# Performance work log

Measured on AMD Instinct MI355X. Metric: run time of the kernel, lower is better.

The kernel has to match this reference:

```python
import jax, jax.numpy as jnp
import numpy as np

B, H, W = 8, 64, 64
C = 256
NUM_HEADS = 8
HEAD_DIM = C // NUM_HEADS  # 32
K0, K1 = 7, 13  # two neighborhood kernel sizes (dilation = 1)


def _starts(L, K):
    """NATTEN (dilation=1) window start and relative-bias start per position."""
    nh = K // 2
    i = jnp.arange(L)
    win = jnp.maximum(i - nh, 0) + jnp.where(i + nh >= L, L - i - nh - 1, 0)
    pb = nh + jnp.where(i < nh, nh - i, 0) + jnp.where(i + nh >= L, L - i - 1 - nh, 0)
    return win, pb


def _na2d(q, k, v, rpb, K):
    """2D neighborhood attention with relative positional bias.
    q,k,v: [B,h,H,W,D] (q pre-scaled); rpb: [h, 2K-1, 2K-1]."""
    Bq, h, Hq, Wq, D = q.shape
    sh, ph = _starts(Hq, K)
    sw, pw = _starts(Wq, K)
    kk = jnp.arange(K)
    idx_h = sh[:, None] + kk            # [H,K] neighbor row indices
    idx_w = sw[:, None] + kk            # [W,K] neighbor col indices
    rows = ph[:, None] + kk             # [H,K] rpb row offsets
    cols = pw[:, None] + kk             # [W,K] rpb col offsets
    # bias[hd,i,ki,j,kj] = rpb[hd, rows[i,ki], cols[j,kj]] -> [h,H,K,W,K]
    bias = rpb[:, rows[:, :, None, None], cols[None, None, :, :]]
    bias = bias.transpose(0, 1, 3, 2, 4)  # [h,H,W,K,K]
    # QK: loop over the K kernel rows (small fixed set) to avoid a [B,h,H,K,W,K,D] blowup
    attn_rows = []
    for ki in range(K):
        kh = jnp.take(k, idx_h[:, ki], axis=2)      # [B,h,H,W,D]
        khw = jnp.take(kh, idx_w, axis=3)           # [B,h,H,W,K,D]
        attn_rows.append(jnp.einsum('bhijd,bhijkd->bhijk', q, khw))
    attn = jnp.stack(attn_rows, axis=4)             # [B,h,H,W,K,K]
    attn = attn + bias[None]
    attn = jax.nn.softmax(attn.reshape(Bq, h, Hq, Wq, K * K), axis=-1)
    attn = attn.reshape(Bq, h, Hq, Wq, K, K)
    # AV: same row-wise gather
    out = jnp.zeros_like(q)
    for ki in range(K):
        vh = jnp.take(v, idx_h[:, ki], axis=2)      # [B,h,H,W,D]
        vhw = jnp.take(vh, idx_w, axis=3)           # [B,h,H,W,K,D]
        out = out + jnp.einsum('bhijk,bhijkd->bhijd', attn[:, :, :, :, ki, :], vhw)
    return out


def setup_inputs() -> dict:
    key = jax.random.key(0)
    ks = jax.random.split(key, 7)
    x = jax.random.normal(ks[0], (B, H, W, C), dtype=jnp.float32)
    w_qkv = jax.random.normal(ks[1], (3 * C, C), dtype=jnp.float32) * 0.02
    b_qkv = jnp.zeros((3 * C,), dtype=jnp.float32)
    rpb0 = jnp.clip(jax.random.normal(ks[2], (NUM_HEADS // 2, 2 * K0 - 1, 2 * K0 - 1), dtype=jnp.float32) * 0.02, -2.0, 2.0)
    rpb1 = jnp.clip(jax.random.normal(ks[3], (NUM_HEADS // 2, 2 * K1 - 1, 2 * K1 - 1), dtype=jnp.float32) * 0.02, -2.0, 2.0)
    w_proj = jax.random.normal(ks[4], (C, C), dtype=jnp.float32) * 0.02
    b_proj = jnp.zeros((C,), dtype=jnp.float32)
    return {"x": x, "w_qkv": w_qkv, "b_qkv": b_qkv, "rpb0": rpb0, "rpb1": rpb1,
            "w_proj": w_proj, "b_proj": b_proj}


def reference(x, w_qkv, b_qkv, rpb0, rpb1, w_proj, b_proj):
    Bx, Hx, Wx, Cx = x.shape
    nh, hd = NUM_HEADS, Cx // NUM_HEADS
    qkv = (x @ w_qkv.T + b_qkv).reshape(Bx, Hx, Wx, 3, nh, hd)
    qkv = qkv.transpose(3, 0, 4, 1, 2, 5)           # [3,B,nh,H,W,hd]
    q, k, v = qkv[0], qkv[1], qkv[2]
    q = q * (hd ** -0.5)
    half = nh // 2
    x0 = _na2d(q[:, :half], k[:, :half], v[:, :half], rpb0, K0)
    x1 = _na2d(q[:, half:], k[:, half:], v[:, half:], rpb1, K1)
    y = jnp.concatenate([x0, x1], axis=1)           # [B,nh,H,W,hd]
    y = y.transpose(0, 2, 3, 1, 4).reshape(Bx, Hx, Wx, Cx)
    return y @ w_proj.T + b_proj
```

## Files before the change

kernel.cpp:

```cpp
#include <hip/hip_runtime.h>
#include <hip/hip_bf16.h>

typedef __attribute__((ext_vector_type(8))) short short8;
typedef __attribute__((ext_vector_type(4))) float f32x4;

#define GM 32768
#define DH 32
#define LOG2E 1.4426950408889634f

__device__ __forceinline__ ushort f2bf(float f) {
  unsigned int u = __float_as_uint(f);
  u += 0x7FFFu + ((u >> 16) & 1u);
  return (ushort)(u >> 16);
}
__device__ __forceinline__ unsigned int cvtpk(float a, float b) {
  unsigned int r;
  asm("v_cvt_pk_bf16_f32 %0, %1, %2" : "=v"(r) : "v"(a), "v"(b));
  return r;
}

template<int MODE>
__global__ __launch_bounds__(256) void gemm_bt(
    const float* __restrict__ Af, const ushort* __restrict__ Ab,
    const float* __restrict__ Bf,
    ushort* __restrict__ Cb, float* __restrict__ Cf, const float* __restrict__ bias,
    float scale) {
  const int BM = 128, BN = 128, BK = 64, K = 256;
  __shared__ int4 sA4[BM * BK / 8];
  __shared__ int4 sB4[BN * BK / 8];

  int id = blockIdx.x;
  int xcd = id & 7, rest = id >> 3;
  int bm, bn;
  if (MODE == 0) { bm = xcd * 32 + rest / 6;    bn = rest % 6; }
  else           { bm = xcd * 32 + (rest >> 1); bn = rest & 1; }

  int tid = threadIdx.x;
  int lane = tid & 63, wid = tid >> 6;
  int wm = (wid >> 1) * 64, wn = (wid & 1) * 64;
  int lo = lane & 15, hi = lane >> 4;

  f32x4 acc[4][4] = {};

  for (int kt = 0; kt < K; kt += BK) {
    int4 ra[4], rb[4];
#pragma unroll
    for (int i = 0; i < 4; ++i) {
      int cid = tid + i * 256;
      int r = cid >> 3, c = cid & 7;
      if (MODE == 0) {
        const float* p = Af + (size_t)(bm * BM + r) * K + kt + c * 8;
        float4 t0 = *(const float4*)p, t1 = *(const float4*)(p + 4);
        ra[i] = make_int4(cvtpk(t0.x, t0.y), cvtpk(t0.z, t0.w),
                          cvtpk(t1.x, t1.y), cvtpk(t1.z, t1.w));
      } else {
        ra[i] = *(const int4*)(Ab + (size_t)(bm * BM + r) * K + kt + c * 8);
      }
      const float* q = Bf + (size_t)(bn * BN + r) * K + kt + c * 8;
      float4 s0 = *(const float4*)q, s1 = *(const float4*)(q + 4);
      rb[i] = make_int4(cvtpk(s0.x, s0.y), cvtpk(s0.z, s0.w),
                        cvtpk(s1.x, s1.y), cvtpk(s1.z, s1.w));
    }
    __syncthreads();
#pragma unroll
    for (int i = 0; i < 4; ++i) {
      int cid = tid + i * 256;
      int r = cid >> 3, c = cid & 7;
      sA4[r * 8 + (c ^ (r & 7))] = ra[i];
      sB4[r * 8 + (c ^ (r & 7))] = rb[i];
    }
    __syncthreads();
#pragma unroll
    for (int ks = 0; ks < 2; ++ks) {
      short8 af[4], bfr[4];
#pragma unroll
      for (int mi = 0; mi < 4; ++mi) {
        int r = wm + mi * 16 + lo, c = ks * 4 + hi;
        af[mi] = ((const short8*)sA4)[r * 8 + (c ^ (r & 7))];
      }
#pragma unroll
      for (int nj = 0; nj < 4; ++nj) {
        int r = wn + nj * 16 + lo, c = ks * 4 + hi;
        bfr[nj] = ((const short8*)sB4)[r * 8 + (c ^ (r & 7))];
      }
#pragma unroll
      for (int mi = 0; mi < 4; ++mi)
#pragma unroll
        for (int nj = 0; nj < 4; ++nj)
          acc[mi][nj] = __builtin_amdgcn_mfma_f32_16x16x32_bf16(
              af[mi], bfr[nj], acc[mi][nj], 0, 0, 0);
    }
  }

  if (MODE == 0) {
    float sc = (bn < 2) ? scale : 1.0f;
    __syncthreads();
    ushort* sC = (ushort*)sA4;
#pragma unroll
    for (int mi = 0; mi < 4; ++mi)
#pragma unroll
      for (int nj = 0; nj < 4; ++nj)
#pragma unroll
        for (int r = 0; r < 4; ++r) {
          int row = wm + mi * 16 + hi * 4 + r;
          int col = wn + nj * 16 + lo;
          float v = (acc[mi][nj][r] + bias[bn * BN + col]) * sc;
          sC[row * 128 + (((col >> 3) ^ (row & 15)) << 3) + (col & 7)] = f2bf(v);
        }
    __syncthreads();
    int sel = bn >> 1;
    size_t base0 = ((size_t)(sel * 8 + (bn & 1) * 4) * GM + (size_t)bm * BM) * DH;
#pragma unroll
    for (int p8 = 0; p8 < 8; ++p8) {
      int o = p8 * 256 + tid;
      int hh = o >> 9, row = (o >> 2) & 127, q = o & 3;
      int4 val = *(const int4*)(sC + row * 128 + (((hh * 4 + q) ^ (row & 15)) << 3));
      *(int4*)(Cb + base0 + (size_t)hh * GM * DH + row * DH + q * 8) = val;
    }
  } else {
#pragma unroll
    for (int mi = 0; mi < 4; ++mi)
#pragma unroll
      for (int nj = 0; nj < 4; ++nj)
#pragma unroll
        for (int r = 0; r < 4; ++r) {
          int row = bm * BM + wm + mi * 16 + hi * 4 + r;
          int col = bn * BN + wn + nj * 16 + lo;
          Cf[(size_t)row * 256 + col] = acc[mi][nj][r] + bias[col];
        }
  }
}

__global__ __launch_bounds__(256) void transpose_v(const ushort* __restrict__ vsrc,
                                                   ushort* __restrict__ vt) {
  __shared__ ushort tile[DH][264];
  int hb = blockIdx.x >> 7;
  int pb = (blockIdx.x & 127) << 8;
  int t = threadIdx.x;
  const ushort* src = vsrc + ((size_t)hb * GM + pb + t) * DH;
  short8 rbuf[4];
#pragma unroll
  for (int c4 = 0; c4 < 4; ++c4) rbuf[c4] = *(const short8*)(src + c4 * 8);
#pragma unroll
  for (int c4 = 0; c4 < 4; ++c4)
#pragma unroll
    for (int e = 0; e < 8; ++e)
      tile[c4 * 8 + e][t] = (ushort)rbuf[c4][e];
  __syncthreads();
  int d = t >> 3, seg = t & 7;
  ushort* dst = vt + ((size_t)hb * DH + d) * GM + pb + seg * 32;
  const ushort* srow = &tile[d][seg * 32];
#pragma unroll
  for (int c4 = 0; c4 < 4; ++c4)
    *(short8*)(dst + c4 * 8) = *(const short8*)(srow + c4 * 8);
}

template<int KS>
__device__ __forceinline__ void natt_row(const ushort* __restrict__ qkvb,
                                         const ushort* __restrict__ vt,
                                         const float* __restrict__ rpb,
                                         ushort* __restrict__ y,
                                         float* sbias, unsigned int* sP,
                                         int b, int hl, int h, int i) {
  const int NHF = KS / 2, BW = 2 * KS - 1, LK = 64 - KS;
  int tid = threadIdx.x;
  int lane = tid & 63, w = tid >> 6, lo = lane & 15, hi = lane >> 4;

  int wi = i - NHF; wi = wi < 0 ? 0 : (wi > LK ? LK : wi);
  int pi = NHF + ((i < NHF) ? (NHF - i) : 0) + ((i >= 64 - NHF) ? (63 - NHF - i) : 0);

  for (int t = tid; t < 2 * KS * BW; t += 256) {
    float v;
    if (t < KS * BW) {
      int ki = t / BW, cb = t - ki * BW;
      v = rpb[((size_t)hl * BW + pi + ki) * BW + cb] * LOG2E;
    } else v = -1e30f;
    sbias[t] = v;
  }
  __syncthreads();

  const ushort* qb = qkvb;
  const ushort* kb = qkvb + (size_t)8 * GM * DH;

  int jbase = 16 * w;
  int j = jbase + lo;
  size_t posQ = (size_t)h * GM + b * 4096 + i * 64 + j;
  short8 aq = *(const short8*)(qb + posQ * DH + hi * 8);

  int wj16 = jbase - NHF; wj16 = wj16 < 0 ? 0 : (wj16 > LK ? LK : wj16);
  int cbase = wj16 < 32 ? wj16 : 32;
  int wj = j - NHF; wj = wj < 0 ? 0 : (wj > LK ? LK : wj);

  int aoff[8];
#pragma unroll
  for (int t = 0; t < 8; ++t) {
    int c = cbase + (t >> 2) * 16 + hi * 4 + (t & 3);
    int idx = c - j + (KS - 1);
    bool valid = (c >= wj) && (c < wj + KS);
    aoff[t] = valid ? idx * 4 : KS * BW * 4;
  }

  unsigned int* sPw = sP + w * 640;
  unsigned int* pw1 = sPw + lo * 20 + 2 * hi;
  unsigned int* pw2 = sPw + lo * 20 + 8 + 2 * hi;
  const unsigned int* pr = sPw + lo * 20 + 4 * hi;

  const char* sb = (const char*)sbias;
  const ushort* kband = kb + ((size_t)h * GM + b * 4096 + (size_t)wi * 64 + cbase) * DH;
  const ushort* vrow0 = vt + ((size_t)h * DH + lo) * GM
                        + ((size_t)b * 4096 + (size_t)wi * 64 + cbase + hi * 8);
  const ushort* vrow1 = vrow0 + (size_t)16 * GM;

#define LOADK(KI, F0, F1) { const ushort* kr_ = kband + (KI) * 64 * DH; \
    F0 = *(const short8*)(kr_ + lo * DH + hi * 8); \
    F1 = *(const short8*)(kr_ + (16 + lo) * DH + hi * 8); }
#define LOADV(KI, F0, F1) { \
    F0 = *(const short8*)(vrow0 + (KI) * 64); \
    F1 = *(const short8*)(vrow1 + (KI) * 64); }

  const f32x4 zero = {};
  f32x4 o0 = {}, o1 = {};
  float den0 = 0.f, den1 = 0.f;

  short8 ck0, ck1, cv0, cv1, nk0, nk1, nv0, nv1, vp0, vp1;
  LOADK(0, ck0, ck1);
  LOADV(0, cv0, cv1);

#pragma unroll
  for (int ki = 0; ki < KS; ++ki) {
    if (ki + 1 < KS) {
      LOADK(ki + 1, nk0, nk1);
      LOADV(ki + 1, nv0, nv1);
    }
    f32x4 s0 = __builtin_amdgcn_mfma_f32_16x16x32_bf16(ck0, aq, zero, 0, 0, 0);
    f32x4 s1 = __builtin_amdgcn_mfma_f32_16x16x32_bf16(ck1, aq, zero, 0, 0, 0);
    float p[8];
#pragma unroll
    for (int t = 0; t < 8; ++t) {
      float bv = *(const float*)(sb + (aoff[t] + ki * BW * 4));
      float sv = (t < 4) ? s0[t & 3] : s1[t & 3];
      float e;
      asm("v_exp_f32 %0, %1" : "=v"(e) : "v"(sv + bv));
      p[t] = e;
      if (t & 1) den1 += e; else den0 += e;
    }
    unsigned int u0 = cvtpk(p[0], p[1]), u1 = cvtpk(p[2], p[3]);
    unsigned int u2 = cvtpk(p[4], p[5]), u3 = cvtpk(p[6], p[7]);
    *(uint2*)(pw1 + (ki & 1) * 320) = make_uint2(u0, u1);
    *(uint2*)(pw2 + (ki & 1) * 320) = make_uint2(u2, u3);
    if (ki > 0) {
      short8 pa = *(const short8*)(pr + ((ki - 1) & 1) * 320);
      o0 = __builtin_amdgcn_mfma_f32_16x16x32_bf16(pa, vp0, o0, 0, 0, 0);
      o1 = __builtin_amdgcn_mfma_f32_16x16x32_bf16(pa, vp1, o1, 0, 0, 0);
    }
    vp0 = cv0; vp1 = cv1;
    cv0 = nv0; cv1 = nv1;
    ck0 = nk0; ck1 = nk1;
  }
  {
    short8 pa = *(const short8*)(pr + ((KS - 1) & 1) * 320);
    o0 = __builtin_amdgcn_mfma_f32_16x16x32_bf16(pa, vp0, o0, 0, 0, 0);
    o1 = __builtin_amdgcn_mfma_f32_16x16x32_bf16(pa, vp1, o1, 0, 0, 0);
  }
#undef LOADK
#undef LOADV

  float den = den0 + den1;
  den += __shfl_xor(den, 16);
  den += __shfl_xor(den, 32);
  float inv = 1.f / den;
  float dinv[4];
#pragma unroll
  for (int r = 0; r < 4; ++r) dinv[r] = __shfl(inv, hi * 4 + r);

  size_t ybase = ((size_t)b * 4096 + (size_t)i * 64 + jbase) * 256 + h * DH;
#pragma unroll
  for (int r = 0; r < 4; ++r) {
    int jr = hi * 4 + r;
    y[ybase + (size_t)jr * 256 + lo]      = f2bf(o0[r] * dinv[r]);
    y[ybase + (size_t)jr * 256 + 16 + lo] = f2bf(o1[r] * dinv[r]);
  }
}

__global__ __launch_bounds__(256) void natt_mfma(const ushort* __restrict__ qkvb,
    const ushort* __restrict__ vt, const float* __restrict__ rpb0,
    const float* __restrict__ rpb1, ushort* __restrict__ y) {
  __shared__ float sbias[2 * 13 * 25];
  __shared__ unsigned int sP[4 * 640];
  int blk = blockIdx.x;
  int xcd = blk & 7, rest = blk >> 3;
  int b = rest >> 6, i = rest & 63;
  int ho = (xcd - b) & 7;
  if (ho < 4) natt_row<13>(qkvb, vt, rpb1, y, sbias, sP, b, ho, ho + 4, i);
  else        natt_row<7> (qkvb, vt, rpb0, y, sbias, sP, b, ho - 4, ho - 4, i);
}

extern "C" void kernel_launch(void* const* d_in, const int* in_sizes, int n_in,
                              void* d_out, int out_size, void* d_ws, size_t ws_size,
                              hipStream_t stream) {
  const float* x      = (const float*)d_in[0];
  const float* w_qkv  = (const float*)d_in[1];
  const float* b_qkv  = (const float*)d_in[2];
  const float* rpb0   = (const float*)d_in[3];
  const float* rpb1   = (const float*)d_in[4];
  const float* w_proj = (const float*)d_in[5];
  const float* b_proj = (const float*)d_in[6];
  float* out = (float*)d_out;

  char* ws = (char*)d_ws;
  ushort* qkvb = (ushort*)(ws);
  ushort* vt   = (ushort*)(ws + (48u << 20));
  ushort* yb   = (ushort*)(ws + (64u << 20));

  gemm_bt<0><<<1536, 256, 0, stream>>>(x, nullptr, w_qkv, qkvb, nullptr, b_qkv,
                                       0.17677669529663687f * LOG2E);
  transpose_v<<<1024, 256, 0, stream>>>(qkvb + (size_t)16 * GM * DH, vt);
  natt_mfma<<<4096, 256, 0, stream>>>(qkvb, vt, rpb0, rpb1, yb);
  gemm_bt<1><<<512, 256, 0, stream>>>(nullptr, yb, w_proj, nullptr, out, b_proj, 1.0f);
}
```

Measured before the change: 234.6 us.

## Fuse V transpose into QKV GEMM epilogue and process query row pairs

The QKV GEMM epilogue now writes the V tiles straight into the transposed layout through shared memory, which removes the separate transpose kernel and its round trip of V through global memory. The neighborhood attention kernel now handles two adjacent query rows per block. They share one sweep over the K/V key rows, so each key and value row is loaded once and used by both queries, and the grid is halved. In exchange, the loop has a runtime trip count with more branches, and the kernel uses more registers and LDS. The strided per-element LDS reads in the transposed epilogue may cause bank conflicts.

Measured after the change: 198.4 us. -15.4%, faster.

```diff
diff --git a/kernel.cpp b/kernel.cpp
--- a/kernel.cpp
+++ b/kernel.cpp
@@ -23,11 +23,12 @@
 __global__ __launch_bounds__(256) void gemm_bt(
     const float* __restrict__ Af, const ushort* __restrict__ Ab,
     const float* __restrict__ Bf,
-    ushort* __restrict__ Cb, float* __restrict__ Cf, const float* __restrict__ bias,
-    float scale) {
+    ushort* __restrict__ Cb, ushort* __restrict__ Vt,
+    float* __restrict__ Cf, const float* __restrict__ bias, float scale) {
   const int BM = 128, BN = 128, BK = 64, K = 256;
-  __shared__ int4 sA4[BM * BK / 8];
-  __shared__ int4 sB4[BN * BK / 8];
+  __shared__ int4 sAB[2 * BM * BK / 8];
+  int4* sA4 = sAB;
+  int4* sB4 = sAB + BM * BK / 8;
 
   int id = blockIdx.x;
   int xcd = id & 7, rest = id >> 3;
@@ -95,7 +96,7 @@
   if (MODE == 0) {
     float sc = (bn < 2) ? scale : 1.0f;
     __syncthreads();
-    ushort* sC = (ushort*)sA4;
+    ushort* sC = (ushort*)sAB;
 #pragma unroll
     for (int mi = 0; mi < 4; ++mi)
 #pragma unroll
@@ -108,14 +109,31 @@
           sC[row * 128 + (((col >> 3) ^ (row & 15)) << 3) + (col & 7)] = f2bf(v);
         }
     __syncthreads();
-    int sel = bn >> 1;
-    size_t base0 = ((size_t)(sel * 8 + (bn & 1) * 4) * GM + (size_t)bm * BM) * DH;
-#pragma unroll
-    for (int p8 = 0; p8 < 8; ++p8) {
-      int o = p8 * 256 + tid;
-      int hh = o >> 9, row = (o >> 2) & 127, q = o & 3;
-      int4 val = *(const int4*)(sC + row * 128 + (((hh * 4 + q) ^ (row & 15)) << 3));
-      *(int4*)(Cb + base0 + (size_t)hh * GM * DH + row * DH + q * 8) = val;
+    if (bn < 4) {
+      int sel = bn >> 1;
+      size_t base0 = ((size_t)(sel * 8 + (bn & 1) * 4) * GM + (size_t)bm * BM) * DH;
+#pragma unroll
+      for (int p8 = 0; p8 < 8; ++p8) {
+        int o = p8 * 256 + tid;
+        int hh = o >> 9, row = (o >> 2) & 127, q = o & 3;
+        int4 val = *(const int4*)(sC + row * 128 + (((hh * 4 + q) ^ (row & 15)) << 3));
+        *(int4*)(Cb + base0 + (size_t)hh * GM * DH + row * DH + q * 8) = val;
+      }
+    } else {
+      int hb32 = (bn - 4) * 128;
+#pragma unroll
+      for (int p8 = 0; p8 < 8; ++p8) {
+        int o = p8 * 256 + tid;
+        int col = o >> 4, chunk = o & 15;
+        int4 val;
+        ushort* vp = (ushort*)&val;
+#pragma unroll
+        for (int e = 0; e < 8; ++e) {
+          int row = chunk * 8 + e;
+          vp[e] = sC[row * 128 + (((col >> 3) ^ (row & 15)) << 3) + (col & 7)];
+        }
+        *(int4*)(Vt + (size_t)(hb32 + col) * GM + (size_t)bm * BM + chunk * 8) = val;
+      }
     }
   } else {
 #pragma unroll
@@ -131,50 +149,33 @@
   }
 }
 
-__global__ __launch_bounds__(256) void transpose_v(const ushort* __restrict__ vsrc,
-                                                   ushort* __restrict__ vt) {
-  __shared__ ushort tile[DH][264];
-  int hb = blockIdx.x >> 7;
-  int pb = (blockIdx.x & 127) << 8;
-  int t = threadIdx.x;
-  const ushort* src = vsrc + ((size_t)hb * GM + pb + t) * DH;
-  short8 rbuf[4];
-#pragma unroll
-  for (int c4 = 0; c4 < 4; ++c4) rbuf[c4] = *(const short8*)(src + c4 * 8);
-#pragma unroll
-  for (int c4 = 0; c4 < 4; ++c4)
-#pragma unroll
-    for (int e = 0; e < 8; ++e)
-      tile[c4 * 8 + e][t] = (ushort)rbuf[c4][e];
-  __syncthreads();
-  int d = t >> 3, seg = t & 7;
-  ushort* dst = vt + ((size_t)hb * DH + d) * GM + pb + seg * 32;
-  const ushort* srow = &tile[d][seg * 32];
-#pragma unroll
-  for (int c4 = 0; c4 < 4; ++c4)
-    *(short8*)(dst + c4 * 8) = *(const short8*)(srow + c4 * 8);
-}
-
 template<int KS>
-__device__ __forceinline__ void natt_row(const ushort* __restrict__ qkvb,
-                                         const ushort* __restrict__ vt,
-                                         const float* __restrict__ rpb,
-                                         ushort* __restrict__ y,
-                                         float* sbias, unsigned int* sP,
-                                         int b, int hl, int h, int i) {
-  const int NHF = KS / 2, BW = 2 * KS - 1, LK = 64 - KS;
+__device__ __forceinline__ void natt_pair(const ushort* __restrict__ qkvb,
+                                          const ushort* __restrict__ vt,
+                                          const float* __restrict__ rpb,
+                                          ushort* __restrict__ y,
+                                          float* sbias, unsigned int* sP,
+                                          int b, int hl, int h, int i0) {
+  const int NHF = KS / 2, BW = 2 * KS - 1, LK = 64 - KS, TS = KS * BW;
   int tid = threadIdx.x;
   int lane = tid & 63, w = tid >> 6, lo = lane & 15, hi = lane >> 4;
-
-  int wi = i - NHF; wi = wi < 0 ? 0 : (wi > LK ? LK : wi);
-  int pi = NHF + ((i < NHF) ? (NHF - i) : 0) + ((i >= 64 - NHF) ? (63 - NHF - i) : 0);
-
-  for (int t = tid; t < 2 * KS * BW; t += 256) {
-    float v;
-    if (t < KS * BW) {
+  int i1 = i0 + 1;
+
+  int wi0 = i0 - NHF; wi0 = wi0 < 0 ? 0 : (wi0 > LK ? LK : wi0);
+  int wi1 = i1 - NHF; wi1 = wi1 < 0 ? 0 : (wi1 > LK ? LK : wi1);
+  int d = wi1 - wi0;
+  int pi0 = NHF + ((i0 < NHF) ? (NHF - i0) : 0) + ((i0 >= 64 - NHF) ? (63 - NHF - i0) : 0);
+  int pi1 = NHF + ((i1 < NHF) ? (NHF - i1) : 0) + ((i1 >= 64 - NHF) ? (63 - NHF - i1) : 0);
+
+  for (int t = tid; t < 4 * TS; t += 256) {
+    float v = -1e30f;
+    if (t < TS) {
       int ki = t / BW, cb = t - ki * BW;
-      v = rpb[((size_t)hl * BW + pi + ki) * BW + cb] * LOG2E;
-    } else v = -1e30f;
+      v = rpb[((size_t)hl * BW + pi0 + ki) * BW + cb] * LOG2E;
+    } else if (t < 2 * TS) {
+      int tt = t - TS, ki = tt / BW, cb = tt - ki * BW;
+      v = rpb[((size_t)hl * BW + pi1 + ki) * BW + cb] * LOG2E;
+    }
     sbias[t] = v;
   }
   __syncthreads();
@@ -184,8 +185,9 @@
 
   int jbase = 16 * w;
   int j = jbase + lo;
-  size_t posQ = (size_t)h * GM + b * 4096 + i * 64 + j;
-  short8 aq = *(const short8*)(qb + posQ * DH + hi * 8);
+  size_t posQ0 = (size_t)h * GM + b * 4096 + i0 * 64 + j;
+  short8 aq0 = *(const short8*)(qb + posQ0 * DH + hi * 8);
+  short8 aq1 = *(const short8*)(qb + (posQ0 + 64) * DH + hi * 8);
 
   int wj16 = jbase - NHF; wj16 = wj16 < 0 ? 0 : (wj16 > LK ? LK : wj16);
   int cbase = wj16 < 32 ? wj16 : 32;
@@ -197,18 +199,18 @@
     int c = cbase + (t >> 2) * 16 + hi * 4 + (t & 3);
     int idx = c - j + (KS - 1);
     bool valid = (c >= wj) && (c < wj + KS);
-    aoff[t] = valid ? idx * 4 : KS * BW * 4;
-  }
-
-  unsigned int* sPw = sP + w * 640;
-  unsigned int* pw1 = sPw + lo * 20 + 2 * hi;
-  unsigned int* pw2 = sPw + lo * 20 + 8 + 2 * hi;
-  const unsigned int* pr = sPw + lo * 20 + 4 * hi;
+    aoff[t] = valid ? idx * 4 : 2 * TS * 4;
+  }
+  int rbase1 = (TS - d * BW) * 4;
+
+  unsigned int* base0 = sP + (w * 4) * 320;
+  unsigned int* base1 = sP + (w * 4 + 2) * 320;
+  int pwo1 = lo * 20 + 2 * hi, pwo2 = lo * 20 + 8 + 2 * hi, pro = lo * 20 + 4 * hi;
 
   const char* sb = (const char*)sbias;
-  const ushort* kband = kb + ((size_t)h * GM + b * 4096 + (size_t)wi * 64 + cbase) * DH;
+  const ushort* kband = kb + ((size_t)h * GM + b * 4096 + (size_t)wi0 * 64 + cbase) * DH;
   const ushort* vrow0 = vt + ((size_t)h * DH + lo) * GM
-                        + ((size_t)b * 4096 + (size_t)wi * 64 + cbase + hi * 8);
+                        + ((size_t)b * 4096 + (size_t)wi0 * 64 + cbase + hi * 8);
   const ushort* vrow1 = vrow0 + (size_t)16 * GM;
 
 #define LOADK(KI, F0, F1) { const ushort* kr_ = kband + (KI) * 64 * DH; \
@@ -219,80 +221,101 @@
     F1 = *(const short8*)(vrow1 + (KI) * 64); }
 
   const f32x4 zero = {};
-  f32x4 o0 = {}, o1 = {};
-  float den0 = 0.f, den1 = 0.f;
+  f32x4 o0_0 = {}, o1_0 = {}, o0_1 = {}, o1_1 = {};
+  float dena0 = 0.f, denb0 = 0.f, dena1 = 0.f, denb1 = 0.f;
 
   short8 ck0, ck1, cv0, cv1, nk0, nk1, nv0, nv1, vp0, vp1;
   LOADK(0, ck0, ck1);
   LOADV(0, cv0, cv1);
-
-#pragma unroll
-  for (int ki = 0; ki < KS; ++ki) {
-    if (ki + 1 < KS) {
-      LOADK(ki + 1, nk0, nk1);
-      LOADV(ki + 1, nv0, nv1);
-    }
-    f32x4 s0 = __builtin_amdgcn_mfma_f32_16x16x32_bf16(ck0, aq, zero, 0, 0, 0);
-    f32x4 s1 = __builtin_amdgcn_mfma_f32_16x16x32_bf16(ck1, aq, zero, 0, 0, 0);
-    float p[8];
-#pragma unroll
-    for (int t = 0; t < 8; ++t) {
-      float bv = *(const float*)(sb + (aoff[t] + ki * BW * 4));
-      float sv = (t < 4) ? s0[t & 3] : s1[t & 3];
-      float e;
-      asm("v_exp_f32 %0, %1" : "=v"(e) : "v"(sv + bv));
-      p[t] = e;
-      if (t & 1) den1 += e; else den0 += e;
-    }
-    unsigned int u0 = cvtpk(p[0], p[1]), u1 = cvtpk(p[2], p[3]);
-    unsigned int u2 = cvtpk(p[4], p[5]), u3 = cvtpk(p[6], p[7]);
-    *(uint2*)(pw1 + (ki & 1) * 320) = make_uint2(u0, u1);
-    *(uint2*)(pw2 + (ki & 1) * 320) = make_uint2(u2, u3);
-    if (ki > 0) {
-      short8 pa = *(const short8*)(pr + ((ki - 1) & 1) * 320);
-      o0 = __builtin_amdgcn_mfma_f32_16x16x32_bf16(pa, vp0, o0, 0, 0, 0);
-      o1 = __builtin_amdgcn_mfma_f32_16x16x32_bf16(pa, vp1, o1, 0, 0, 0);
+  nk0 = ck0; nk1 = ck1; nv0 = cv0; nv1 = cv1;
+  vp0 = cv0; vp1 = cv1;
+
+  int tend = KS + d;
+  for (int t = 0; t <= tend; ++t) {
+    if (t + 1 < tend) { LOADK(t + 1, nk0, nk1); LOADV(t + 1, nv0, nv1); }
+    int slot = (t & 1) * 320, slotp = ((t - 1) & 1) * 320;
+    int tb = t * BW * 4;
+    if (t < KS) {
+      f32x4 s0 = __builtin_amdgcn_mfma_f32_16x16x32_bf16(ck0, aq0, zero, 0, 0, 0);
+      f32x4 s1 = __builtin_amdgcn_mfma_f32_16x16x32_bf16(ck1, aq0, zero, 0, 0, 0);
+      float p[8];
+#pragma unroll
+      for (int e = 0; e < 8; ++e) {
+        float bv = *(const float*)(sb + (aoff[e] + tb));
+        float sv = (e < 4) ? s0[e & 3] : s1[e & 3];
+        float ex;
+        asm("v_exp_f32 %0, %1" : "=v"(ex) : "v"(sv + bv));
+        p[e] = ex;
+        if (e & 1) denb0 += ex; else dena0 += ex;
+      }
+      *(uint2*)(base0 + slot + pwo1) = make_uint2(cvtpk(p[0], p[1]), cvtpk(p[2], p[3]));
+      *(uint2*)(base0 + slot + pwo2) = make_uint2(cvtpk(p[4], p[5]), cvtpk(p[6], p[7]));
+    }
+    if (t >= d && t < KS + d) {
+      f32x4 s0 = __builtin_amdgcn_mfma_f32_16x16x32_bf16(ck0, aq1, zero, 0, 0, 0);
+      f32x4 s1 = __builtin_amdgcn_mfma_f32_16x16x32_bf16(ck1, aq1, zero, 0, 0, 0);
+      float p[8];
+#pragma unroll
+      for (int e = 0; e < 8; ++e) {
+        float bv = *(const float*)(sb + (aoff[e] + rbase1 + tb));
+        float sv = (e < 4) ? s0[e & 3] : s1[e & 3];
+        float ex;
+        asm("v_exp_f32 %0, %1" : "=v"(ex) : "v"(sv + bv));
+        p[e] = ex;
+        if (e & 1) denb1 += ex; else dena1 += ex;
+      }
+      *(uint2*)(base1 + slot + pwo1) = make_uint2(cvtpk(p[0], p[1]), cvtpk(p[2], p[3]));
+      *(uint2*)(base1 + slot + pwo2) = make_uint2(cvtpk(p[4], p[5]), cvtpk(p[6], p[7]));
+    }
+    if (t >= 1 && t <= KS) {
+      short8 pa = *(const short8*)(base0 + slotp + pro);
+      o0_0 = __builtin_amdgcn_mfma_f32_16x16x32_bf16(pa, vp0, o0_0, 0, 0, 0);
+      o1_0 = __builtin_amdgcn_mfma_f32_16x16x32_bf16(pa, vp1, o1_0, 0, 0, 0);
+    }
+    if (t >= d + 1) {
+      short8 pa = *(const short8*)(base1 + slotp + pro);
+      o0_1 = __builtin_amdgcn_mfma_f32_16x16x32_bf16(pa, vp0, o0_1, 0, 0, 0);
+      o1_1 = __builtin_amdgcn_mfma_f32_16x16x32_bf16(pa, vp1, o1_1, 0, 0, 0);
     }
     vp0 = cv0; vp1 = cv1;
     cv0 = nv0; cv1 = nv1;
     ck0 = nk0; ck1 = nk1;
   }
-  {
-    short8 pa = *(const short8*)(pr + ((KS - 1) & 1) * 320);
-    o0 = __builtin_amdgcn_mfma_f32_16x16x32_bf16(pa, vp0, o0, 0, 0, 0);
-    o1 = __builtin_amdgcn_mfma_f32_16x16x32_bf16(pa, vp1, o1, 0, 0, 0);
-  }
 #undef LOADK
 #undef LOADV
 
-  float den = den0 + den1;
-  den += __shfl_xor(den, 16);
-  den += __shfl_xor(den, 32);
-  float inv = 1.f / den;
-  float dinv[4];
-#pragma unroll
-  for (int r = 0; r < 4; ++r) dinv[r] = __shfl(inv, hi * 4 + r);
-
-  size_t ybase = ((size_t)b * 4096 + (size_t)i * 64 + jbase) * 256 + h * DH;
-#pragma unroll
-  for (int r = 0; r < 4; ++r) {
-    int jr = hi * 4 + r;
-    y[ybase + (size_t)jr * 256 + lo]      = f2bf(o0[r] * dinv[r]);
-    y[ybase + (size_t)jr * 256 + 16 + lo] = f2bf(o1[r] * dinv[r]);
+#pragma unroll
+  for (int r = 0; r < 2; ++r) {
+    float den = (r == 0) ? (dena0 + denb0) : (dena1 + denb1);
+    den += __shfl_xor(den, 16);
+    den += __shfl_xor(den, 32);
+    float inv = 1.f / den;
+    float dinv[4];
+#pragma unroll
+    for (int q = 0; q < 4; ++q) dinv[q] = __shfl(inv, hi * 4 + q);
+    f32x4 oa = (r == 0) ? o0_0 : o0_1;
+    f32x4 ob = (r == 0) ? o1_0 : o1_1;
+    size_t ybase = ((size_t)b * 4096 + (size_t)(i0 + r) * 64 + jbase) * 256 + h * DH;
+#pragma unroll
+    for (int q = 0; q < 4; ++q) {
+      int jr = hi * 4 + q;
+      y[ybase + (size_t)jr * 256 + lo]      = f2bf(oa[q] * dinv[q]);
+      y[ybase + (size_t)jr * 256 + 16 + lo] = f2bf(ob[q] * dinv[q]);
+    }
   }
 }
 
 __global__ __launch_bounds__(256) void natt_mfma(const ushort* __restrict__ qkvb,
     const ushort* __restrict__ vt, const float* __restrict__ rpb0,
     const float* __restrict__ rpb1, ushort* __restrict__ y) {
-  __shared__ float sbias[2 * 13 * 25];
-  __shared__ unsigned int sP[4 * 640];
+  __shared__ float sbias[4 * 13 * 25];
+  __shared__ unsigned int sP[4 * 4 * 320];
   int blk = blockIdx.x;
   int xcd = blk & 7, rest = blk >> 3;
-  int b = rest >> 6, i = rest & 63;
+  int b = rest >> 5, i0 = (rest & 31) * 2;
   int ho = (xcd - b) & 7;
-  if (ho < 4) natt_row<13>(qkvb, vt, rpb1, y, sbias, sP, b, ho, ho + 4, i);
-  else        natt_row<7> (qkvb, vt, rpb0, y, sbias, sP, b, ho - 4, ho - 4, i);
+  if (ho < 4) natt_pair<13>(qkvb, vt, rpb1, y, sbias, sP, b, ho, ho + 4, i0);
+  else        natt_pair<7> (qkvb, vt, rpb0, y, sbias, sP, b, ho - 4, ho - 4, i0);
 }
 
 extern "C" void kernel_launch(void* const* d_in, const int* in_sizes, int n_in,
@@ -309,12 +332,12 @@
 
   char* ws = (char*)d_ws;
   ushort* qkvb = (ushort*)(ws);
-  ushort* vt   = (ushort*)(ws + (48u << 20));
-  ushort* yb   = (ushort*)(ws + (64u << 20));
-
-  gemm_bt<0><<<1536, 256, 0, stream>>>(x, nullptr, w_qkv, qkvb, nullptr, b_qkv,
+  ushort* vt   = (ushort*)(ws + (32u << 20));
+  ushort* yb   = (ushort*)(ws + (48u << 20));
+
+  gemm_bt<0><<<1536, 256, 0, stream>>>(x, nullptr, w_qkv, qkvb, vt, nullptr, b_qkv,
                                        0.17677669529663687f * LOG2E);
-  transpose_v<<<1024, 256, 0, stream>>>(qkvb + (size_t)16 * GM * DH, vt);
-  natt_mfma<<<4096, 256, 0, stream>>>(qkvb, vt, rpb0, rpb1, yb);
-  gemm_bt<1><<<512, 256, 0, stream>>>(nullptr, yb, w_proj, nullptr, out, b_proj, 1.0f);
-}
+  natt_mfma<<<2048, 256, 0, stream>>>(qkvb, vt, rpb0, rpb1, yb);
+  gemm_bt<1><<<512, 256, 0, stream>>>(nullptr, yb, w_proj, nullptr, nullptr, out,
+                                      b_proj, 1.0f);
+}
```
